# Optimization experiments

Hardware: AMD Instinct MI355X
Metric: run time of the kernel (lower is better)

Reference implementation:

```python
import jax, jax.numpy as jnp
import numpy as np

ALPHA = 0.5  # smooth_quant migration strength
N_TOKENS, D_MODEL = 32768, 1024  # square linear: d_in == d_out (required by diag_s @ weight)


def setup_inputs() -> dict:
    key = jax.random.key(0)
    k1, k2, k3 = jax.random.split(key, 3)
    x = jax.random.normal(k1, (N_TOKENS, D_MODEL), dtype=jnp.float32)
    weight = jax.random.normal(k2, (D_MODEL, D_MODEL), dtype=jnp.float32) * 0.02
    bias = jax.random.normal(k3, (D_MODEL,), dtype=jnp.float32) * 0.02
    return {"x": x, "weight": weight, "bias": bias}


def reference(x, weight, bias):
    # SmoothQuant rescale: per-in-channel maxima of activations and weight.
    max_act = jnp.max(x, axis=0) ** ALPHA                 # [D]
    max_w = jnp.max(weight, axis=0) ** (1.0 - ALPHA)      # [D] (max over out dim -> per in-channel)
    s = max_act / max_w                                   # [D] scale_fact
    # x_hat = x @ diag(s)^-1 ; expressed as the equivalent per-channel broadcast.
    x_hat = x / s                                         # [N, D]
    # weight_hat = diag(s) @ weight (square linear, row rescale).
    w_hat = s[:, None] * weight                           # [D, D]
    # nn.Linear forward: x_hat @ weight_hat^T + bias
    return x_hat @ w_hat.T + bias
```

## Files before the change

### kernel.cpp

```cpp
#include <hip/hip_runtime.h>
#include <hip/hip_bf16.h>
#include <stdint.h>

#define D_MODEL 1024

typedef __attribute__((ext_vector_type(4))) float  f32x4;
typedef __attribute__((ext_vector_type(8))) __bf16 bf16x8;
typedef __attribute__((ext_vector_type(8))) unsigned short u16x8;
typedef __attribute__((ext_vector_type(4))) unsigned short u16x4;


__device__ __forceinline__ unsigned order_map(float x) {
    unsigned u = __float_as_uint(x);
    return (u & 0x80000000u) ? ~u : (u | 0x80000000u);
}
__device__ __forceinline__ float order_unmap(unsigned m) {
    unsigned b = (m & 0x80000000u) ? (m & 0x7fffffffu) : ~m;
    return __uint_as_float(b);
}
__device__ __forceinline__ unsigned short f2bf(float f) {
    unsigned u = __float_as_uint(f);
    u += 0x7fffu + ((u >> 16) & 1u);
    return (unsigned short)(u >> 16);
}


__global__ void init_u32(unsigned* __restrict__ p, int n) {
    int i = blockIdx.x * blockDim.x + threadIdx.x;
    if (i < n) p[i] = 0u;
}

__global__ void colmax_kernel(const float* __restrict__ src, int rows_per_slab,
                              int cols, unsigned* __restrict__ out_u) {
    int k = blockIdx.x * blockDim.x + threadIdx.x;
    const float* p = src + (size_t)blockIdx.y * rows_per_slab * cols + k;
    float m = -__builtin_inff();
#pragma unroll 4
    for (int r = 0; r < rows_per_slab; ++r)
        m = fmaxf(m, p[(size_t)r * cols]);
    atomicMax(&out_u[k], order_map(m));
}

#define CC_ROWS 16
__global__ __launch_bounds__(256)
void colmax_convert(const float* __restrict__ x,
                    float* __restrict__ partial,
                    unsigned short* __restrict__ xb) {
    int c4 = threadIdx.x * 4;
    size_t base = (size_t)blockIdx.x * CC_ROWS * D_MODEL + c4;
    f32x4 m4 = {-__builtin_inff(), -__builtin_inff(), -__builtin_inff(), -__builtin_inff()};
#pragma unroll 8
    for (int r = 0; r < CC_ROWS; ++r) {
        f32x4 v = *reinterpret_cast<const f32x4*>(&x[base + (size_t)r * D_MODEL]);
        u16x4 o;
#pragma unroll
        for (int e = 0; e < 4; ++e) { m4[e] = fmaxf(m4[e], v[e]); o[e] = f2bf(v[e]); }
        *reinterpret_cast<u16x4*>(&xb[base + (size_t)r * D_MODEL]) = o;
    }
    *reinterpret_cast<f32x4*>(&partial[(size_t)blockIdx.x * D_MODEL + c4]) = m4;
}

__global__ void reduce_partial(const float* __restrict__ partial,
                               unsigned* __restrict__ ma_u) {
    int col  = blockIdx.x * 256 + threadIdx.x;
    int b0   = blockIdx.y * 64;
    float m = -__builtin_inff();
#pragma unroll 8
    for (int i = 0; i < 64; ++i)
        m = fmaxf(m, partial[(size_t)(b0 + i) * D_MODEL + col]);
    atomicMax(&ma_u[col], order_map(m));
}

__global__ void scale_kernel(const unsigned* __restrict__ ma_u,
                             const unsigned* __restrict__ mw_u,
                             float* __restrict__ s) {
    int k = blockIdx.x * blockDim.x + threadIdx.x;
    if (k < D_MODEL) {
        float ma = order_unmap(ma_u[k]);
        float mw = order_unmap(mw_u[k]);
        s[k] = sqrtf(ma) / sqrtf(mw);
    }
}

__global__ void build_w_kernel(const float* __restrict__ W, const float* __restrict__ s,
                               unsigned short* __restrict__ Wp) {
    int j  = blockIdx.x;
    int k4 = threadIdx.x * 4;
    float sj = s[j];
    f32x4 w  = *reinterpret_cast<const f32x4*>(&W[(size_t)j * D_MODEL + k4]);
    f32x4 sk = *reinterpret_cast<const f32x4*>(&s[k4]);
    u16x4 o;
#pragma unroll
    for (int i = 0; i < 4; ++i) o[i] = f2bf(sj * w[i] / sk[i]);
    *reinterpret_cast<u16x4*>(&Wp[(size_t)j * D_MODEL + k4]) = o;
}

#define GBM 256
#define GBN 256
#define GBK 32
#define GNT (D_MODEL / GBK)
#define BUF_SHORTS 8192

__global__ __launch_bounds__(512, 2)
void gemm_main(const unsigned short* __restrict__ Xb,
               const unsigned short* __restrict__ Wp,
               const float* __restrict__ bias,
               float* __restrict__ out) {
    __shared__ __align__(16) unsigned short lds[6 * BUF_SHORTS];

    int flat  = blockIdx.x;
    int xcd   = flat & 7;
    int j     = flat >> 3;
    int col0  = (j & 3) * GBN;
    int row0  = ((xcd << 4) + (j >> 2)) * GBM;

    int tid  = threadIdx.x;
    int wave = tid >> 6;
    int lane = tid & 63;
    int wr   = wave >> 2;
    int wc   = wave & 3;
    int l16  = lane & 15;
    int lq   = lane >> 4;

    int sline = lane >> 3;
    int slog  = (lane & 7) ^ sline;
    int sh    = slog >> 2;
    int sq    = slog & 3;

    f32x4 acc[8][4];
#pragma unroll
    for (int m = 0; m < 8; ++m)
#pragma unroll
        for (int n = 0; n < 4; ++n)
            acc[m][n] = (f32x4){0.f, 0.f, 0.f, 0.f};

    auto stage = [&](int t, int b) {
        int k0 = t * GBK;
#pragma unroll
        for (int r = 0; r < 2; ++r) {
            int line = r * 64 + wave * 8 + sline;
            const unsigned short* gA =
                Xb + (size_t)(row0 + 2 * line + sh) * D_MODEL + k0 + sq * 8;
            __builtin_amdgcn_global_load_lds(
                (const __attribute__((address_space(1))) void*)gA,
                (__attribute__((address_space(3))) void*)&lds[b * BUF_SHORTS + line * 64],
                16, 0, 0);
            const unsigned short* gB =
                Wp + (size_t)(col0 + 2 * line + sh) * D_MODEL + k0 + sq * 8;
            __builtin_amdgcn_global_load_lds(
                (const __attribute__((address_space(1))) void*)gB,
                (__attribute__((address_space(3))) void*)&lds[(3 + b) * BUF_SHORTS + line * 64],
                16, 0, 0);
        }
    };

    stage(0, 0);
    stage(1, 1);

    int cur = 0;
#pragma unroll 1
    for (int t = 0; t < GNT; ++t) {
        if (t + 1 < GNT) asm volatile("s_waitcnt vmcnt(4)" ::: "memory");
        else             asm volatile("s_waitcnt vmcnt(0)" ::: "memory");
        __builtin_amdgcn_s_barrier();

        if (t + 2 < GNT) {
            int bnext = cur >= 1 ? cur - 1 : cur + 2;
            stage(t + 2, bnext);
        }

        const char* Ab = (const char*)&lds[cur * BUF_SHORTS];
        const char* Bb = (const char*)&lds[(3 + cur) * BUF_SHORTS];

        bf16x8 bfr[4];
#pragma unroll
        for (int n = 0; n < 4; ++n) {
            int cc   = wc * 64 + n * 16 + l16;
            int line = cc >> 1;
            int o    = (((cc & 1) << 6) + (lq << 4)) ^ ((line & 7) << 4);
            bfr[n] = *reinterpret_cast<const bf16x8*>(Bb + line * 128 + o);
        }
        bf16x8 afr[8];
#pragma unroll
        for (int m = 0; m < 8; ++m) {
            int rr   = wr * 128 + m * 16 + l16;
            int line = rr >> 1;
            int o    = (((rr & 1) << 6) + (lq << 4)) ^ ((line & 7) << 4);
            afr[m] = *reinterpret_cast<const bf16x8*>(Ab + line * 128 + o);
        }

        __builtin_amdgcn_s_setprio(1);
#pragma unroll
        for (int m = 0; m < 8; ++m)
#pragma unroll
            for (int n = 0; n < 4; ++n)
                acc[m][n] = __builtin_amdgcn_mfma_f32_16x16x32_bf16(
                    afr[m], bfr[n], acc[m][n], 0, 0, 0);
        __builtin_amdgcn_s_setprio(0);

        cur = cur == 2 ? 0 : cur + 1;
    }

    int crow = row0 + wr * 128;
    int ccol = col0 + wc * 64;
#pragma unroll
    for (int n = 0; n < 4; ++n) {
        int col = ccol + n * 16 + l16;
        float b = bias[col];
#pragma unroll
        for (int m = 0; m < 8; ++m) {
            int r = crow + m * 16 + lq * 4;
#pragma unroll
            for (int q = 0; q < 4; ++q)
                out[(size_t)(r + q) * D_MODEL + col] = acc[m][n][q] + b;
        }
    }
}

__global__ __launch_bounds__(256)
void gemm_fallback(const float* __restrict__ X, const unsigned short* __restrict__ Wp,
                   const float* __restrict__ bias, float* __restrict__ out, int N) {
    __shared__ __align__(16) unsigned short As[128][64];
    __shared__ __align__(16) unsigned short Bs[128][64];

    int flat = blockIdx.x;
    int swz  = ((gridDim.x & 7) == 0)
             ? (flat & 7) * (gridDim.x >> 3) + (flat >> 3) : flat;
    const int nColBlk = D_MODEL / 128;
    int row0 = (swz / nColBlk) * 128;
    int col0 = (swz % nColBlk) * 128;

    int tid  = threadIdx.x;
    int wave = tid >> 6;
    int lane = tid & 63;
    int wr   = wave >> 1;
    int wc   = wave & 1;
    int l16  = lane & 15;
    int srow  = lane >> 3;
    int skoff = ((lane & 7) ^ srow) << 3;

    f32x4 acc[4][4];
#pragma unroll
    for (int m = 0; m < 4; ++m)
#pragma unroll
        for (int n = 0; n < 4; ++n)
            acc[m][n] = (f32x4){0.f, 0.f, 0.f, 0.f};

    for (int k0 = 0; k0 < D_MODEL; k0 += 64) {
        __syncthreads();
#pragma unroll
        for (int i = 0; i < 4; ++i) {
            int c   = i * 256 + tid;
            int r   = c >> 3;
            int seg = c & 7;
            const float* gp = X + (size_t)(row0 + r) * D_MODEL + k0 + seg * 8;
            f32x4 x0 = *reinterpret_cast<const f32x4*>(gp);
            f32x4 x1 = *reinterpret_cast<const f32x4*>(gp + 4);
            u16x8 v;
#pragma unroll
            for (int e = 0; e < 4; ++e) { v[e] = f2bf(x0[e]); v[e + 4] = f2bf(x1[e]); }
            int off = (seg * 16) ^ ((r & 7) << 4);
            *reinterpret_cast<u16x8*>((char*)&As[0][0] + r * 128 + off) = v;
        }
#pragma unroll
        for (int i = 0; i < 4; ++i) {
            int r0 = (wave * 4 + i) * 8;
            const unsigned short* g = Wp + (size_t)(col0 + r0 + srow) * D_MODEL + k0 + skoff;
            __builtin_amdgcn_global_load_lds(
                (const __attribute__((address_space(1))) void*)g,
                (__attribute__((address_space(3))) void*)&Bs[r0][0], 16, 0, 0);
        }
        __syncthreads();
#pragma unroll
        for (int kk = 0; kk < 2; ++kk) {
            bf16x8 af[4], bf_[4];
#pragma unroll
            for (int m = 0; m < 4; ++m) {
                int row = wr * 64 + m * 16 + l16;
                int o   = ((lane >> 4) * 16 + kk * 64) ^ ((row & 7) << 4);
                af[m] = *reinterpret_cast<const bf16x8*>((const char*)&As[0][0] + row * 128 + o);
            }
#pragma unroll
            for (int n = 0; n < 4; ++n) {
                int row = wc * 64 + n * 16 + l16;
                int o   = ((lane >> 4) * 16 + kk * 64) ^ ((row & 7) << 4);
                bf_[n] = *reinterpret_cast<const bf16x8*>((const char*)&Bs[0][0] + row * 128 + o);
            }
#pragma unroll
            for (int m = 0; m < 4; ++m)
#pragma unroll
                for (int n = 0; n < 4; ++n)
                    acc[m][n] = __builtin_amdgcn_mfma_f32_16x16x32_bf16(
                        af[m], bf_[n], acc[m][n], 0, 0, 0);
        }
    }

    int crow = row0 + wr * 64;
    int ccol = col0 + wc * 64;
#pragma unroll
    for (int n = 0; n < 4; ++n) {
        int col = ccol + n * 16 + l16;
        float b = bias[col];
#pragma unroll
        for (int m = 0; m < 4; ++m) {
            int r = crow + m * 16 + (lane >> 4) * 4;
#pragma unroll
            for (int q = 0; q < 4; ++q)
                out[(size_t)(r + q) * D_MODEL + col] = acc[m][n][q] + b;
        }
    }
}


extern "C" void kernel_launch(void* const* d_in, const int* in_sizes, int n_in,
                              void* d_out, int out_size, void* d_ws, size_t ws_size,
                              hipStream_t stream) {
    const float* x    = (const float*)d_in[0];
    const float* w    = (const float*)d_in[1];
    const float* bias = (const float*)d_in[2];
    float* out        = (float*)d_out;
    const int N       = in_sizes[0] / D_MODEL;

    char* ws               = (char*)d_ws;
    unsigned*       ma_u   = (unsigned*)(ws);
    unsigned*       mw_u   = (unsigned*)(ws + 4096);
    float*          s      = (float*)(ws + 8192);
    unsigned short* Wp     = (unsigned short*)(ws + 16384);
    unsigned short* Xb     = (unsigned short*)(ws + 16384 + (size_t)D_MODEL * D_MODEL * 2);
    const int nPart        = N / CC_ROWS;
    float*          part   = (float*)(ws + 16384 + (size_t)D_MODEL * D_MODEL * 2
                                               + (size_t)N * D_MODEL * 2);

    size_t need = 16384 + (size_t)D_MODEL * D_MODEL * 2 + (size_t)N * D_MODEL * 2
                + (size_t)nPart * D_MODEL * 4;
    bool preconv = ws_size >= need;

    init_u32<<<8, 256, 0, stream>>>((unsigned*)ws, 2048);

    if (preconv) {
        colmax_convert<<<nPart, 256, 0, stream>>>(x, part, Xb);
        reduce_partial<<<dim3(D_MODEL / 256, nPart / 64), 256, 0, stream>>>(part, ma_u);
    } else {
        colmax_kernel<<<dim3(D_MODEL / 256, 64), 256, 0, stream>>>(x, N / 64, D_MODEL, ma_u);
    }
    colmax_kernel<<<dim3(D_MODEL / 256, 16), 256, 0, stream>>>(w, D_MODEL / 16, D_MODEL, mw_u);
    scale_kernel<<<D_MODEL / 256, 256, 0, stream>>>(ma_u, mw_u, s);
    build_w_kernel<<<D_MODEL, 256, 0, stream>>>(w, s, Wp);

    if (preconv) {
        int nblk = (N / GBM) * (D_MODEL / GBN);
        gemm_main<<<nblk, 512, 0, stream>>>(Xb, Wp, bias, out);
    } else {
        int nblk = (N / 128) * (D_MODEL / 128);
        gemm_fallback<<<nblk, 256, 0, stream>>>(x, Wp, bias, out, N);
    }
}
```

Before: 154.0 us.

## Fuse fp32-to-bf16 activation conversion into GEMM A-tile loading

The separate pre-pass that wrote a bf16 copy of x is dropped; the column-max kernel now only reads x. The GEMM loads fp32 activation tiles into registers two steps ahead, converts them to bf16 and stores them swizzled into LDS, while W still streams through direct global-to-LDS loads. This removes a full bf16 write and re-read of the activation matrix, at the cost of the GEMM reading fp32 A four times (once per column block), plus extra register pressure and conversion ALU work inside the main loop.

```diff
diff --git a/kernel.cpp b/kernel.cpp
--- a/kernel.cpp
+++ b/kernel.cpp
@@ -43,19 +43,15 @@
 
 #define CC_ROWS 16
 __global__ __launch_bounds__(256)
-void colmax_convert(const float* __restrict__ x,
-                    float* __restrict__ partial,
-                    unsigned short* __restrict__ xb) {
+void colmax_part(const float* __restrict__ x, float* __restrict__ partial) {
     int c4 = threadIdx.x * 4;
     size_t base = (size_t)blockIdx.x * CC_ROWS * D_MODEL + c4;
     f32x4 m4 = {-__builtin_inff(), -__builtin_inff(), -__builtin_inff(), -__builtin_inff()};
 #pragma unroll 8
     for (int r = 0; r < CC_ROWS; ++r) {
         f32x4 v = *reinterpret_cast<const f32x4*>(&x[base + (size_t)r * D_MODEL]);
-        u16x4 o;
-#pragma unroll
-        for (int e = 0; e < 4; ++e) { m4[e] = fmaxf(m4[e], v[e]); o[e] = f2bf(v[e]); }
-        *reinterpret_cast<u16x4*>(&xb[base + (size_t)r * D_MODEL]) = o;
+#pragma unroll
+        for (int e = 0; e < 4; ++e) m4[e] = fmaxf(m4[e], v[e]);
     }
     *reinterpret_cast<f32x4*>(&partial[(size_t)blockIdx.x * D_MODEL + c4]) = m4;
 }
@@ -102,7 +98,7 @@
 #define BUF_SHORTS 8192
 
 __global__ __launch_bounds__(512, 2)
-void gemm_main(const unsigned short* __restrict__ Xb,
+void gemm_main(const float* __restrict__ X,
                const unsigned short* __restrict__ Wp,
                const float* __restrict__ bias,
                float* __restrict__ out) {
@@ -121,11 +117,16 @@
     int wc   = wave & 3;
     int l16  = lane & 15;
     int lq   = lane >> 4;
-
     int sline = lane >> 3;
     int slog  = (lane & 7) ^ sline;
     int sh    = slog >> 2;
     int sq    = slog & 3;
+    int ar   = tid >> 1;
+    int akh  = (tid & 1) * 16;
+    int aline = tid >> 2;
+    int as0   = (((tid >> 1) & 1) << 2) | ((tid & 1) << 1);
+    int aoff0 = aline * 128 + (((as0    ) << 4) ^ ((aline & 7) << 4));
+    int aoff1 = aline * 128 + (((as0 + 1) << 4) ^ ((aline & 7) << 4));
 
     f32x4 acc[8][4];
 #pragma unroll
@@ -134,43 +135,56 @@
         for (int n = 0; n < 4; ++n)
             acc[m][n] = (f32x4){0.f, 0.f, 0.f, 0.f};
 
-    auto stage = [&](int t, int b) {
+    f32x4 apf0[4], apf1[4];
+
+    auto issueA = [&](int t, f32x4 (&apf)[4]) {
+        const float* gp = X + (size_t)(row0 + ar) * D_MODEL + t * GBK + akh;
+#pragma unroll
+        for (int i = 0; i < 4; ++i)
+            apf[i] = *reinterpret_cast<const f32x4*>(gp + i * 4);
+    };
+    auto issueB = [&](int t, int b) {
         int k0 = t * GBK;
 #pragma unroll
         for (int r = 0; r < 2; ++r) {
             int line = r * 64 + wave * 8 + sline;
-            const unsigned short* gA =
-                Xb + (size_t)(row0 + 2 * line + sh) * D_MODEL + k0 + sq * 8;
-            __builtin_amdgcn_global_load_lds(
-                (const __attribute__((address_space(1))) void*)gA,
-                (__attribute__((address_space(3))) void*)&lds[b * BUF_SHORTS + line * 64],
-                16, 0, 0);
-            const unsigned short* gB =
+            const unsigned short* g =
                 Wp + (size_t)(col0 + 2 * line + sh) * D_MODEL + k0 + sq * 8;
             __builtin_amdgcn_global_load_lds(
-                (const __attribute__((address_space(1))) void*)gB,
+                (const __attribute__((address_space(1))) void*)g,
                 (__attribute__((address_space(3))) void*)&lds[(3 + b) * BUF_SHORTS + line * 64],
                 16, 0, 0);
         }
     };
-
-    stage(0, 0);
-    stage(1, 1);
-
-    int cur = 0;
-#pragma unroll 1
-    for (int t = 0; t < GNT; ++t) {
-        if (t + 1 < GNT) asm volatile("s_waitcnt vmcnt(4)" ::: "memory");
-        else             asm volatile("s_waitcnt vmcnt(0)" ::: "memory");
-        __builtin_amdgcn_s_barrier();
-
-        if (t + 2 < GNT) {
-            int bnext = cur >= 1 ? cur - 1 : cur + 2;
-            stage(t + 2, bnext);
-        }
-
-        const char* Ab = (const char*)&lds[cur * BUF_SHORTS];
-        const char* Bb = (const char*)&lds[(3 + cur) * BUF_SHORTS];
+    auto convA = [&](f32x4 (&apf)[4], int b) {
+        u16x8 v0, v1;
+#pragma unroll
+        for (int e = 0; e < 4; ++e) {
+            v0[e]     = f2bf(apf[0][e]);
+            v0[e + 4] = f2bf(apf[1][e]);
+            v1[e]     = f2bf(apf[2][e]);
+            v1[e + 4] = f2bf(apf[3][e]);
+        }
+        char* ab = (char*)&lds[b * BUF_SHORTS];
+        *reinterpret_cast<u16x8*>(ab + aoff0) = v0;
+        *reinterpret_cast<u16x8*>(ab + aoff1) = v1;
+    };
+
+    issueA(0, apf0); issueB(0, 0);
+    issueA(1, apf1); issueB(1, 1);
+    convA(apf0, 0);
+    asm volatile("s_waitcnt vmcnt(8)" ::: "memory");
+    asm volatile("s_waitcnt lgkmcnt(0)" ::: "memory");
+    __builtin_amdgcn_s_barrier();
+
+    int c0 = 0, c1 = 1, c2 = 2;
+
+    auto body = [&](int t, f32x4 (&cur)[4], f32x4 (&nxt)[4]) {
+        if (t + 2 < GNT) { issueA(t + 2, cur); issueB(t + 2, c2); }
+        if (t + 1 < GNT) convA(nxt, c1);
+
+        const char* Ab = (const char*)&lds[c0 * BUF_SHORTS];
+        const char* Bb = (const char*)&lds[(3 + c0) * BUF_SHORTS];
 
         bf16x8 bfr[4];
 #pragma unroll
@@ -198,7 +212,19 @@
                     afr[m], bfr[n], acc[m][n], 0, 0, 0);
         __builtin_amdgcn_s_setprio(0);
 
-        cur = cur == 2 ? 0 : cur + 1;
+        if (t + 1 < GNT) {
+            if (t + 2 < GNT) asm volatile("s_waitcnt vmcnt(8)" ::: "memory");
+            else             asm volatile("s_waitcnt vmcnt(0)" ::: "memory");
+            asm volatile("s_waitcnt lgkmcnt(0)" ::: "memory");
+            __builtin_amdgcn_s_barrier();
+        }
+        int tmp = c0; c0 = c1; c1 = c2; c2 = tmp;
+    };
+
+#pragma unroll 1
+    for (int tt = 0; tt < GNT; tt += 2) {
+        body(tt,     apf0, apf1);
+        body(tt + 1, apf1, apf0);
     }
 
     int crow = row0 + wr * 128;
@@ -210,100 +236,6 @@
 #pragma unroll
         for (int m = 0; m < 8; ++m) {
             int r = crow + m * 16 + lq * 4;
-#pragma unroll
-            for (int q = 0; q < 4; ++q)
-                out[(size_t)(r + q) * D_MODEL + col] = acc[m][n][q] + b;
-        }
-    }
-}
-
-__global__ __launch_bounds__(256)
-void gemm_fallback(const float* __restrict__ X, const unsigned short* __restrict__ Wp,
-                   const float* __restrict__ bias, float* __restrict__ out, int N) {
-    __shared__ __align__(16) unsigned short As[128][64];
-    __shared__ __align__(16) unsigned short Bs[128][64];
-
-    int flat = blockIdx.x;
-    int swz  = ((gridDim.x & 7) == 0)
-             ? (flat & 7) * (gridDim.x >> 3) + (flat >> 3) : flat;
-    const int nColBlk = D_MODEL / 128;
-    int row0 = (swz / nColBlk) * 128;
-    int col0 = (swz % nColBlk) * 128;
-
-    int tid  = threadIdx.x;
-    int wave = tid >> 6;
-    int lane = tid & 63;
-    int wr   = wave >> 1;
-    int wc   = wave & 1;
-    int l16  = lane & 15;
-    int srow  = lane >> 3;
-    int skoff = ((lane & 7) ^ srow) << 3;
-
-    f32x4 acc[4][4];
-#pragma unroll
-    for (int m = 0; m < 4; ++m)
-#pragma unroll
-        for (int n = 0; n < 4; ++n)
-            acc[m][n] = (f32x4){0.f, 0.f, 0.f, 0.f};
-
-    for (int k0 = 0; k0 < D_MODEL; k0 += 64) {
-        __syncthreads();
-#pragma unroll
-        for (int i = 0; i < 4; ++i) {
-            int c   = i * 256 + tid;
-            int r   = c >> 3;
-            int seg = c & 7;
-            const float* gp = X + (size_t)(row0 + r) * D_MODEL + k0 + seg * 8;
-            f32x4 x0 = *reinterpret_cast<const f32x4*>(gp);
-            f32x4 x1 = *reinterpret_cast<const f32x4*>(gp + 4);
-            u16x8 v;
-#pragma unroll
-            for (int e = 0; e < 4; ++e) { v[e] = f2bf(x0[e]); v[e + 4] = f2bf(x1[e]); }
-            int off = (seg * 16) ^ ((r & 7) << 4);
-            *reinterpret_cast<u16x8*>((char*)&As[0][0] + r * 128 + off) = v;
-        }
-#pragma unroll
-        for (int i = 0; i < 4; ++i) {
-            int r0 = (wave * 4 + i) * 8;
-            const unsigned short* g = Wp + (size_t)(col0 + r0 + srow) * D_MODEL + k0 + skoff;
-            __builtin_amdgcn_global_load_lds(
-                (const __attribute__((address_space(1))) void*)g,
-                (__attribute__((address_space(3))) void*)&Bs[r0][0], 16, 0, 0);
-        }
-        __syncthreads();
-#pragma unroll
-        for (int kk = 0; kk < 2; ++kk) {
-            bf16x8 af[4], bf_[4];
-#pragma unroll
-            for (int m = 0; m < 4; ++m) {
-                int row = wr * 64 + m * 16 + l16;
-                int o   = ((lane >> 4) * 16 + kk * 64) ^ ((row & 7) << 4);
-                af[m] = *reinterpret_cast<const bf16x8*>((const char*)&As[0][0] + row * 128 + o);
-            }
-#pragma unroll
-            for (int n = 0; n < 4; ++n) {
-                int row = wc * 64 + n * 16 + l16;
-                int o   = ((lane >> 4) * 16 + kk * 64) ^ ((row & 7) << 4);
-                bf_[n] = *reinterpret_cast<const bf16x8*>((const char*)&Bs[0][0] + row * 128 + o);
-            }
-#pragma unroll
-            for (int m = 0; m < 4; ++m)
-#pragma unroll
-                for (int n = 0; n < 4; ++n)
-                    acc[m][n] = __builtin_amdgcn_mfma_f32_16x16x32_bf16(
-                        af[m], bf_[n], acc[m][n], 0, 0, 0);
-        }
-    }
-
-    int crow = row0 + wr * 64;
-    int ccol = col0 + wc * 64;
-#pragma unroll
-    for (int n = 0; n < 4; ++n) {
-        int col = ccol + n * 16 + l16;
-        float b = bias[col];
-#pragma unroll
-        for (int m = 0; m < 4; ++m) {
-            int r = crow + m * 16 + (lane >> 4) * 4;
 #pragma unroll
             for (int q = 0; q < 4; ++q)
                 out[(size_t)(r + q) * D_MODEL + col] = acc[m][n][q] + b;
@@ -326,19 +258,16 @@
     unsigned*       mw_u   = (unsigned*)(ws + 4096);
     float*          s      = (float*)(ws + 8192);
     unsigned short* Wp     = (unsigned short*)(ws + 16384);
-    unsigned short* Xb     = (unsigned short*)(ws + 16384 + (size_t)D_MODEL * D_MODEL * 2);
     const int nPart        = N / CC_ROWS;
-    float*          part   = (float*)(ws + 16384 + (size_t)D_MODEL * D_MODEL * 2
-                                               + (size_t)N * D_MODEL * 2);
-
-    size_t need = 16384 + (size_t)D_MODEL * D_MODEL * 2 + (size_t)N * D_MODEL * 2
-                + (size_t)nPart * D_MODEL * 4;
-    bool preconv = ws_size >= need;
+    float*          part   = (float*)(ws + 16384 + (size_t)D_MODEL * D_MODEL * 2);
+
+    size_t need = 16384 + (size_t)D_MODEL * D_MODEL * 2 + (size_t)nPart * D_MODEL * 4;
+    bool use_part = ws_size >= need;
 
     init_u32<<<8, 256, 0, stream>>>((unsigned*)ws, 2048);
 
-    if (preconv) {
-        colmax_convert<<<nPart, 256, 0, stream>>>(x, part, Xb);
+    if (use_part) {
+        colmax_part<<<nPart, 256, 0, stream>>>(x, part);
         reduce_partial<<<dim3(D_MODEL / 256, nPart / 64), 256, 0, stream>>>(part, ma_u);
     } else {
         colmax_kernel<<<dim3(D_MODEL / 256, 64), 256, 0, stream>>>(x, N / 64, D_MODEL, ma_u);
@@ -347,11 +276,6 @@
     scale_kernel<<<D_MODEL / 256, 256, 0, stream>>>(ma_u, mw_u, s);
     build_w_kernel<<<D_MODEL, 256, 0, stream>>>(w, s, Wp);
 
-    if (preconv) {
-        int nblk = (N / GBM) * (D_MODEL / GBN);
-        gemm_main<<<nblk, 512, 0, stream>>>(Xb, Wp, bias, out);
-    } else {
-        int nblk = (N / 128) * (D_MODEL / 128);
-        gemm_fallback<<<nblk, 256, 0, stream>>>(x, Wp, bias, out, N);
-    }
-}
+    int nblk = (N / GBM) * (D_MODEL / GBN);
+    gemm_main<<<nblk, 512, 0, stream>>>(x, Wp, bias, out);
+}
```

Result: slower. 171.5 us (+11.4%).
